# Kernel optimization log

Measured on AMD Instinct MI355X. Metric: run time of the kernel, lower is better.

Reference implementation:

```python
import jax, jax.numpy as jnp
import numpy as np

N = 100000
E = 1_600_000
IN_DIM = 128
HIDDEN = 128


def spmm(row, col, vals, H):
    # y[r] = sum_{edges e with row[e]==r} vals[e] * H[col[e]]
    msgs = vals[:, None] * H[col]          # [E, hidden] gather + scale
    return jax.ops.segment_sum(msgs, row, num_segments=H.shape[0])


def setup_inputs() -> dict:
    key = jax.random.key(0)
    ks = jax.random.split(key, 10)
    X = jax.random.normal(ks[0], (N, IN_DIM), dtype=jnp.float32)
    row = jax.random.randint(ks[1], (E,), 0, N, dtype=jnp.int32)
    col = jax.random.randint(ks[2], (E,), 0, N, dtype=jnp.int32)
    vals = jax.random.uniform(ks[3], (E,), dtype=jnp.float32)
    s_in = 1.0 / np.sqrt(IN_DIM)
    s_h = 1.0 / np.sqrt(HIDDEN)
    W_in = jax.random.normal(ks[4], (IN_DIM, HIDDEN), dtype=jnp.float32) * s_in
    b_in = jax.random.normal(ks[5], (HIDDEN,), dtype=jnp.float32) * s_in
    W_mp1 = jax.random.normal(ks[6], (HIDDEN, HIDDEN), dtype=jnp.float32) * s_h
    W_mp2 = jax.random.normal(ks[7], (HIDDEN, HIDDEN), dtype=jnp.float32) * s_h
    W_out = jax.random.normal(ks[8], (HIDDEN, 1), dtype=jnp.float32) * s_h
    b_out = jax.random.normal(ks[9], (1,), dtype=jnp.float32) * s_h
    return {"X": X, "row": row, "col": col, "vals": vals,
            "W_in": W_in, "b_in": b_in, "W_mp1": W_mp1, "W_mp2": W_mp2,
            "W_out": W_out, "b_out": b_out}


def reference(X, row, col, vals, W_in, b_in, W_mp1, W_mp2, W_out, b_out):
    H = jax.nn.relu(X @ W_in + b_in)          # [N, hidden]
    AH = spmm(row, col, vals, H)              # 1-hop propagation
    A2H = spmm(row, col, vals, AH)            # 2-hop propagation
    H2 = jax.nn.relu(AH @ W_mp1 + A2H @ W_mp2)
    return H2 @ W_out + b_out                 # [N, 1]
```

## Files before the change

### kernel.cpp

```cpp
#include <hip/hip_runtime.h>

#define N_NODES 100000
#define N_EDGES 1600000
#define NBUCK 391
#define NCHUNK 256
#define CHUNK 6250
#define LROW 136
#define DCAP 5120

typedef float f32x4 __attribute__((ext_vector_type(4)));
typedef _Float16 f16x8 __attribute__((ext_vector_type(8)));
typedef _Float16 h16x2 __attribute__((ext_vector_type(2)));

__device__ __forceinline__ unsigned f2h_bits(float f) {
    union { _Float16 h; unsigned short s; } c;
    c.h = (_Float16)f;
    return c.s;
}
__device__ __forceinline__ h16x2 u2h(unsigned u) {
    union { unsigned u; h16x2 h; } c;
    c.u = u;
    return c.h;
}
__device__ __forceinline__ unsigned pk16lo(unsigned hi, unsigned lo) {
    return __builtin_amdgcn_perm(hi, lo, 0x05040100u);
}
__device__ __forceinline__ unsigned pk16hi(unsigned hi, unsigned lo) {
    return __builtin_amdgcn_perm(hi, lo, 0x07060302u);
}
__device__ __forceinline__ float fdot2(h16x2 a, h16x2 b, float c) {
#if __has_builtin(__builtin_amdgcn_fdot2)
    return __builtin_amdgcn_fdot2(a, b, c, false);
#else
    return c + (float)a[0] * (float)b[0] + (float)a[1] * (float)b[1];
#endif
}

__device__ __forceinline__ f16x8 pack_h8(float4 a, float4 b) {
    f16x8 r;
    r[0] = (_Float16)a.x; r[1] = (_Float16)a.y;
    r[2] = (_Float16)a.z; r[3] = (_Float16)a.w;
    r[4] = (_Float16)b.x; r[5] = (_Float16)b.y;
    r[6] = (_Float16)b.z; r[7] = (_Float16)b.w;
    return r;
}


__global__ __launch_bounds__(256) void k_prep(const int* __restrict__ row,
                                              int* __restrict__ hmat,
                                              const float* __restrict__ Wa,
                                              const float* __restrict__ Wb,
                                              const float* __restrict__ Wc,
                                              unsigned short* __restrict__ Wta,
                                              unsigned short* __restrict__ Wtb,
                                              unsigned short* __restrict__ Wtc) {
    if (blockIdx.x < NCHUNK) {
        __shared__ int h[NBUCK];
        for (int i = threadIdx.x; i < NBUCK; i += 256) h[i] = 0;
        __syncthreads();
        int s = blockIdx.x * CHUNK, e = s + CHUNK;
        for (int i = s + threadIdx.x; i < e; i += 256)
            atomicAdd(&h[row[i] >> 8], 1);
        __syncthreads();
        for (int b = threadIdx.x; b < NBUCK; b += 256)
            hmat[blockIdx.x * NBUCK + b] = h[b];
    } else {
        int t = (blockIdx.x - NCHUNK) * 256 + threadIdx.x;
        int which = t >> 14;
        int i = t & 16383;
        int n = i & 127, k = i >> 7;
        const float* W = which == 0 ? Wa : which == 1 ? Wb : Wc;
        unsigned short* Wt = which == 0 ? Wta : which == 1 ? Wtb : Wtc;
        Wt[n * 128 + k] = (unsigned short)f2h_bits(W[k * 128 + n]);
    }
}

__global__ __launch_bounds__(512) void k_colscanB(const int* __restrict__ hmat,
                                                  int* __restrict__ bases,
                                                  int* __restrict__ bstart) {
    __shared__ int s[512];
    int b = blockIdx.x, t = threadIdx.x;
    if (b < NBUCK) {
        int v = (t < NCHUNK) ? hmat[t * NBUCK + b] : 0;
        s[t] = v;
        __syncthreads();
        for (int off = 1; off < 512; off <<= 1) {
            int x = (t >= off) ? s[t - off] : 0;
            __syncthreads();
            s[t] += x;
            __syncthreads();
        }
        if (t < NCHUNK) bases[t * NBUCK + b] = s[t] - v;
    } else {
        int v = 0;
        if (t < NBUCK) {
            for (int blk = 0; blk < NCHUNK; blk++) v += hmat[blk * NBUCK + t];
        }
        s[t] = v;
        __syncthreads();
        for (int off = 1; off < 512; off <<= 1) {
            int x = (t >= off) ? s[t - off] : 0;
            __syncthreads();
            s[t] += x;
            __syncthreads();
        }
        if (t < NBUCK) bstart[t] = s[t] - v;
        if (t == NBUCK) bstart[NBUCK] = N_EDGES;
    }
}

__global__ __launch_bounds__(256) void k_binC(const int* __restrict__ row,
                                              const int* __restrict__ col,
                                              const float* __restrict__ vals,
                                              const int* __restrict__ bstart,
                                              const int* __restrict__ bases,
                                              int2* __restrict__ grouped) {
    __shared__ int cnt[NBUCK];
    for (int i = threadIdx.x; i < NBUCK; i += 256) cnt[i] = 0;
    __syncthreads();
    int s = blockIdx.x * CHUNK, e = s + CHUNK;
    for (int i = s + threadIdx.x; i < e; i += 256) {
        int r = row[i];
        int b = r >> 8;
        int rank = atomicAdd(&cnt[b], 1);
        int pos = bstart[b] + bases[blockIdx.x * NBUCK + b] + rank;
        unsigned hv = f2h_bits(vals[i]);
        grouped[pos] = make_int2(col[i], ((r & 255) << 14) | hv);
    }
}

__global__ __launch_bounds__(256) void k_binD(const int2* __restrict__ grouped,
                                              const int* __restrict__ bstart,
                                              unsigned* __restrict__ evf,
                                              int* __restrict__ row_ptr) {
    __shared__ int h[256], sc[256], cur[256];
    __shared__ int2 ebuf[DCAP];
    int b = blockIdx.x, t = threadIdx.x;
    int s0 = bstart[b], e0 = bstart[b + 1];
    int n = e0 - s0;
    bool inlds = (n <= DCAP);
    h[t] = 0;
    __syncthreads();
    if (inlds) {
        for (int i = t; i < n; i += 256) ebuf[i] = grouped[s0 + i];
        __syncthreads();
        for (int i = t; i < n; i += 256)
            atomicAdd(&h[(ebuf[i].y >> 14) & 255], 1);
    } else {
        for (int i = s0 + t; i < e0; i += 256)
            atomicAdd(&h[(grouped[i].y >> 14) & 255], 1);
    }
    __syncthreads();
    int v = h[t];
    sc[t] = v;
    __syncthreads();
    for (int off = 1; off < 256; off <<= 1) {
        int x = (t >= off) ? sc[t - off] : 0;
        __syncthreads();
        sc[t] += x;
        __syncthreads();
    }
    int excl = sc[t] - v;
    cur[t] = excl;
    int grow = b * 256 + t;
    if (grow <= N_NODES) row_ptr[grow] = s0 + excl;
    __syncthreads();
    if (inlds) {
        for (int i = t; i < n; i += 256) {
            int2 g = ebuf[i];
            int rl = (g.y >> 14) & 255;
            int p = atomicAdd(&cur[rl], 1);
            evf[s0 + p] = ((unsigned)g.x << 14) | (unsigned)(g.y & 0x3fff);
        }
    } else {
        for (int i = s0 + t; i < e0; i += 256) {
            int2 g = grouped[i];
            int rl = (g.y >> 14) & 255;
            int p = atomicAdd(&cur[rl], 1);
            evf[s0 + p] = ((unsigned)g.x << 14) | (unsigned)(g.y & 0x3fff);
        }
    }
}

__global__ __launch_bounds__(256) void k_gemm_in(const float* __restrict__ X,
                                                 const unsigned short* __restrict__ Wt,
                                                 const float* __restrict__ b,
                                                 unsigned short* __restrict__ H) {
    __shared__ unsigned short lds[64 * LROW];
    int tid = threadIdx.x;
    int lane = tid & 63, wv = tid >> 6;
    int quad = lane >> 4, c16 = lane & 15;

    f16x8 wf[2][4];
    float bb[2];
#pragma unroll
    for (int nt = 0; nt < 2; nt++) {
        int ng = wv * 2 + nt;
        bb[nt] = b[ng * 16 + c16];
#pragma unroll
        for (int kc = 0; kc < 4; kc++)
            wf[nt][kc] = *(const f16x8*)&Wt[(ng * 16 + c16) * 128 + kc * 32 + quad * 8];
    }

    int tilebase = blockIdx.x * 64;
    const float4* Xg = (const float4*)X;
#pragma unroll
    for (int i = 0; i < 4; i++) {
        int c = tid + i * 256;
        int r = c >> 4, o = c & 15;
        int grow = tilebase + r;
        float4 f0 = make_float4(0.f, 0.f, 0.f, 0.f), f1 = f0;
        if (grow < N_NODES) {
            f0 = Xg[(size_t)grow * 32 + o * 2];
            f1 = Xg[(size_t)grow * 32 + o * 2 + 1];
        }
        *(f16x8*)&lds[r * LROW + o * 8] = pack_h8(f0, f1);
    }
    __syncthreads();

    f32x4 acc[4][2] = {};
#pragma unroll
    for (int t4 = 0; t4 < 4; t4++) {
#pragma unroll
        for (int kc = 0; kc < 4; kc++) {
            f16x8 af = *(const f16x8*)&lds[(t4 * 16 + c16) * LROW + kc * 32 + quad * 8];
#pragma unroll
            for (int nt = 0; nt < 2; nt++)
                acc[t4][nt] = __builtin_amdgcn_mfma_f32_16x16x32_f16(af, wf[nt][kc],
                                                                    acc[t4][nt], 0, 0, 0);
        }
    }
    __syncthreads();

#pragma unroll
    for (int t4 = 0; t4 < 4; t4++)
#pragma unroll
        for (int nt = 0; nt < 2; nt++) {
            int ncol = (wv * 2 + nt) * 16 + c16;
#pragma unroll
            for (int r = 0; r < 4; r++) {
                float v = fmaxf(acc[t4][nt][r] + bb[nt], 0.f);
                lds[(t4 * 16 + quad * 4 + r) * LROW + ncol] = (unsigned short)f2h_bits(v);
            }
        }
    __syncthreads();
#pragma unroll
    for (int i = 0; i < 4; i++) {
        int c = tid + i * 256;
        int r = c >> 4, o = c & 15;
        int grow = tilebase + r;
        if (grow < N_NODES)
            *(uint4*)&H[(size_t)grow * 128 + o * 8] = *(const uint4*)&lds[r * LROW + o * 8];
    }
}

__global__ __launch_bounds__(256) void k_spmm(const int* __restrict__ rp,
                                              const unsigned* __restrict__ evf,
                                              const unsigned* __restrict__ Hin,
                                              unsigned* __restrict__ Ho) {
    int wid = (blockIdx.x * blockDim.x + threadIdx.x) >> 6;
    int lane = threadIdx.x & 63;
    if (wid >= N_NODES) return;
    int q = lane >> 4, l16 = lane & 15;
    int s = __builtin_amdgcn_readfirstlane(rp[wid]);
    int e = __builtin_amdgcn_readfirstlane(rp[wid + 1]);
    float a0 = 0.f, a1 = 0.f, a2 = 0.f, a3 = 0.f;
    float a4 = 0.f, a5 = 0.f, a6 = 0.f, a7 = 0.f;
    for (int base = s; base < e; base += 64) {
        int cnt = e - base;
        if (cnt > 64) cnt = 64;
        unsigned ev = evf[base + (lane < cnt ? lane : cnt - 1)];
        int r = 0;
        for (; r + 16 <= cnt; r += 16) {
            unsigned u0 = __shfl(ev, r + q, 64);
            unsigned u1 = __shfl(ev, r + 4 + q, 64);
            unsigned u2 = __shfl(ev, r + 8 + q, 64);
            unsigned u3 = __shfl(ev, r + 12 + q, 64);
            const uint4 h0 = *(const uint4*)&Hin[(size_t)(u0 >> 14) * 64 + l16 * 4];
            const uint4 h1 = *(const uint4*)&Hin[(size_t)(u1 >> 14) * 64 + l16 * 4];
            const uint4 h2 = *(const uint4*)&Hin[(size_t)(u2 >> 14) * 64 + l16 * 4];
            const uint4 h3 = *(const uint4*)&Hin[(size_t)(u3 >> 14) * 64 + l16 * 4];
            h16x2 v01 = u2h(pk16lo(u1 & 0x3fffu, u0 & 0x3fffu));
            h16x2 v23 = u2h(pk16lo(u3 & 0x3fffu, u2 & 0x3fffu));
            a0 = fdot2(v01, u2h(pk16lo(h1.x, h0.x)), a0);
            a0 = fdot2(v23, u2h(pk16lo(h3.x, h2.x)), a0);
            a1 = fdot2(v01, u2h(pk16hi(h1.x, h0.x)), a1);
            a1 = fdot2(v23, u2h(pk16hi(h3.x, h2.x)), a1);
            a2 = fdot2(v01, u2h(pk16lo(h1.y, h0.y)), a2);
            a2 = fdot2(v23, u2h(pk16lo(h3.y, h2.y)), a2);
            a3 = fdot2(v01, u2h(pk16hi(h1.y, h0.y)), a3);
            a3 = fdot2(v23, u2h(pk16hi(h3.y, h2.y)), a3);
            a4 = fdot2(v01, u2h(pk16lo(h1.z, h0.z)), a4);
            a4 = fdot2(v23, u2h(pk16lo(h3.z, h2.z)), a4);
            a5 = fdot2(v01, u2h(pk16hi(h1.z, h0.z)), a5);
            a5 = fdot2(v23, u2h(pk16hi(h3.z, h2.z)), a5);
            a6 = fdot2(v01, u2h(pk16lo(h1.w, h0.w)), a6);
            a6 = fdot2(v23, u2h(pk16lo(h3.w, h2.w)), a6);
            a7 = fdot2(v01, u2h(pk16hi(h1.w, h0.w)), a7);
            a7 = fdot2(v23, u2h(pk16hi(h3.w, h2.w)), a7);
        }
        if (r < cnt) {
            int i0 = r + q, i1 = r + 4 + q, i2 = r + 8 + q, i3 = r + 12 + q;
            unsigned u0 = __shfl(ev, i0 < cnt ? i0 : cnt - 1, 64);
            unsigned u1 = __shfl(ev, i1 < cnt ? i1 : cnt - 1, 64);
            unsigned u2 = __shfl(ev, i2 < cnt ? i2 : cnt - 1, 64);
            unsigned u3 = __shfl(ev, i3 < cnt ? i3 : cnt - 1, 64);
            const uint4 h0 = *(const uint4*)&Hin[(size_t)(u0 >> 14) * 64 + l16 * 4];
            const uint4 h1 = *(const uint4*)&Hin[(size_t)(u1 >> 14) * 64 + l16 * 4];
            const uint4 h2 = *(const uint4*)&Hin[(size_t)(u2 >> 14) * 64 + l16 * 4];
            const uint4 h3 = *(const uint4*)&Hin[(size_t)(u3 >> 14) * 64 + l16 * 4];
            unsigned m0 = (i0 < cnt) ? (u0 & 0x3fffu) : 0u;
            unsigned m1 = (i1 < cnt) ? (u1 & 0x3fffu) : 0u;
            unsigned m2 = (i2 < cnt) ? (u2 & 0x3fffu) : 0u;
            unsigned m3 = (i3 < cnt) ? (u3 & 0x3fffu) : 0u;
            h16x2 v01 = u2h(pk16lo(m1, m0));
            h16x2 v23 = u2h(pk16lo(m3, m2));
            a0 = fdot2(v01, u2h(pk16lo(h1.x, h0.x)), a0);
            a0 = fdot2(v23, u2h(pk16lo(h3.x, h2.x)), a0);
            a1 = fdot2(v01, u2h(pk16hi(h1.x, h0.x)), a1);
            a1 = fdot2(v23, u2h(pk16hi(h3.x, h2.x)), a1);
            a2 = fdot2(v01, u2h(pk16lo(h1.y, h0.y)), a2);
            a2 = fdot2(v23, u2h(pk16lo(h3.y, h2.y)), a2);
            a3 = fdot2(v01, u2h(pk16hi(h1.y, h0.y)), a3);
            a3 = fdot2(v23, u2h(pk16hi(h3.y, h2.y)), a3);
            a4 = fdot2(v01, u2h(pk16lo(h1.z, h0.z)), a4);
            a4 = fdot2(v23, u2h(pk16lo(h3.z, h2.z)), a4);
            a5 = fdot2(v01, u2h(pk16hi(h1.z, h0.z)), a5);
            a5 = fdot2(v23, u2h(pk16hi(h3.z, h2.z)), a5);
            a6 = fdot2(v01, u2h(pk16lo(h1.w, h0.w)), a6);
            a6 = fdot2(v23, u2h(pk16lo(h3.w, h2.w)), a6);
            a7 = fdot2(v01, u2h(pk16hi(h1.w, h0.w)), a7);
            a7 = fdot2(v23, u2h(pk16hi(h3.w, h2.w)), a7);
        }
    }
    a0 += __shfl_xor(a0, 16, 64); a0 += __shfl_xor(a0, 32, 64);
    a1 += __shfl_xor(a1, 16, 64); a1 += __shfl_xor(a1, 32, 64);
    a2 += __shfl_xor(a2, 16, 64); a2 += __shfl_xor(a2, 32, 64);
    a3 += __shfl_xor(a3, 16, 64); a3 += __shfl_xor(a3, 32, 64);
    a4 += __shfl_xor(a4, 16, 64); a4 += __shfl_xor(a4, 32, 64);
    a5 += __shfl_xor(a5, 16, 64); a5 += __shfl_xor(a5, 32, 64);
    a6 += __shfl_xor(a6, 16, 64); a6 += __shfl_xor(a6, 32, 64);
    a7 += __shfl_xor(a7, 16, 64); a7 += __shfl_xor(a7, 32, 64);
    if (q == 0) {
        uint4 p;
        p.x = (f2h_bits(a1) << 16) | f2h_bits(a0);
        p.y = (f2h_bits(a3) << 16) | f2h_bits(a2);
        p.z = (f2h_bits(a5) << 16) | f2h_bits(a4);
        p.w = (f2h_bits(a7) << 16) | f2h_bits(a6);
        *(uint4*)&Ho[(size_t)wid * 64 + l16 * 4] = p;
    }
}

__global__ __launch_bounds__(256) void k_gemm_out(const unsigned short* __restrict__ AH,
                                                  const unsigned short* __restrict__ A2H,
                                                  const unsigned short* __restrict__ Wt1,
                                                  const unsigned short* __restrict__ Wt2,
                                                  const float* __restrict__ Wout,
                                                  const float* __restrict__ bout,
                                                  float* __restrict__ out) {
    __shared__ unsigned short lds[2][64 * LROW];
    __shared__ float part[4][64];
    int tid = threadIdx.x;
    int lane = tid & 63, wv = tid >> 6;
    int quad = lane >> 4, c16 = lane & 15;

    f16x8 w1f[2][4], w2f[2][4];
    float wo[2];
#pragma unroll
    for (int nt = 0; nt < 2; nt++) {
        int ng = wv * 2 + nt;
        wo[nt] = Wout[ng * 16 + c16];
#pragma unroll
        for (int kc = 0; kc < 4; kc++) {
            w1f[nt][kc] = *(const f16x8*)&Wt1[(ng * 16 + c16) * 128 + kc * 32 + quad * 8];
            w2f[nt][kc] = *(const f16x8*)&Wt2[(ng * 16 + c16) * 128 + kc * 32 + quad * 8];
        }
    }
    float bo = bout[0];

    int tilebase = blockIdx.x * 64;
    const uint4* Ag = (const uint4*)(AH + (size_t)tilebase * 128);
    const uint4* Bg = (const uint4*)(A2H + (size_t)tilebase * 128);
#pragma unroll
    for (int i = 0; i < 4; i++) {
        int c = tid + i * 256;
        int r = c >> 4, o = c & 15;
        *(uint4*)&lds[0][r * LROW + o * 8] = Ag[c];
        *(uint4*)&lds[1][r * LROW + o * 8] = Bg[c];
    }
    __syncthreads();

    f32x4 acc[4][2] = {};
#pragma unroll
    for (int t4 = 0; t4 < 4; t4++) {
#pragma unroll
        for (int kc = 0; kc < 4; kc++) {
            f16x8 afA = *(const f16x8*)&lds[0][(t4 * 16 + c16) * LROW + kc * 32 + quad * 8];
            f16x8 afB = *(const f16x8*)&lds[1][(t4 * 16 + c16) * LROW + kc * 32 + quad * 8];
#pragma unroll
            for (int nt = 0; nt < 2; nt++) {
                acc[t4][nt] = __builtin_amdgcn_mfma_f32_16x16x32_f16(afA, w1f[nt][kc],
                                                                    acc[t4][nt], 0, 0, 0);
                acc[t4][nt] = __builtin_amdgcn_mfma_f32_16x16x32_f16(afB, w2f[nt][kc],
                                                                    acc[t4][nt], 0, 0, 0);
            }
        }
    }

#pragma unroll
    for (int t4 = 0; t4 < 4; t4++) {
        float p[4];
#pragma unroll
        for (int r = 0; r < 4; r++)
            p[r] = fmaxf(acc[t4][0][r], 0.f) * wo[0] + fmaxf(acc[t4][1][r], 0.f) * wo[1];
#pragma unroll
        for (int m = 1; m < 16; m <<= 1)
#pragma unroll
            for (int r = 0; r < 4; r++) p[r] += __shfl_xor(p[r], m, 64);
        if (c16 == 0)
#pragma unroll
            for (int r = 0; r < 4; r++) part[wv][t4 * 16 + quad * 4 + r] = p[r];
    }
    __syncthreads();
    if (tid < 64) {
        int orow = tilebase + tid;
        if (orow < N_NODES)
            out[orow] = part[0][tid] + part[1][tid] + part[2][tid] + part[3][tid] + bo;
    }
}


extern "C" void kernel_launch(void* const* d_in, const int* in_sizes, int n_in,
                              void* d_out, int out_size, void* d_ws, size_t ws_size,
                              hipStream_t stream) {
    const float* X    = (const float*)d_in[0];
    const int*   row  = (const int*)d_in[1];
    const int*   col  = (const int*)d_in[2];
    const float* vals = (const float*)d_in[3];
    const float* W_in = (const float*)d_in[4];
    const float* b_in = (const float*)d_in[5];
    const float* W1   = (const float*)d_in[6];
    const float* W2   = (const float*)d_in[7];
    const float* Wout = (const float*)d_in[8];
    const float* bout = (const float*)d_in[9];
    float* out = (float*)d_out;

    char* ws = (char*)d_ws;
    size_t off = 0;
    auto alloc = [&](size_t bytes) -> void* {
        void* p = ws + off;
        off += (bytes + 511) & ~(size_t)511;
        return p;
    };
    unsigned short* Hb  = (unsigned short*)alloc((size_t)N_NODES * 128 * 2);
    unsigned short* AHb = (unsigned short*)alloc((size_t)N_NODES * 128 * 2);
    unsigned short* A2b = (unsigned short*)alloc((size_t)N_NODES * 128 * 2);
    unsigned* evf  = (unsigned*)alloc((size_t)N_EDGES * 4);
    int2* grouped  = (int2*)alloc((size_t)N_EDGES * 8);
    unsigned short* Wtin = (unsigned short*)alloc(128 * 128 * 2);
    unsigned short* Wt1  = (unsigned short*)alloc(128 * 128 * 2);
    unsigned short* Wt2  = (unsigned short*)alloc(128 * 128 * 2);
    int*   hmat    = (int*)alloc((size_t)NCHUNK * NBUCK * 4);
    int*   bases   = (int*)alloc((size_t)NCHUNK * NBUCK * 4);
    int*   bstart  = (int*)alloc(512 * 4);
    int*   row_ptr = (int*)alloc((size_t)(N_NODES + 256) * 4);

    k_prep<<<NCHUNK + 192, 256, 0, stream>>>(row, hmat, W_in, W1, W2, Wtin, Wt1, Wt2);
    k_colscanB<<<NBUCK + 1, 512, 0, stream>>>(hmat, bases, bstart);
    k_binC<<<NCHUNK, 256, 0, stream>>>(row, col, vals, bstart, bases, grouped);
    k_binD<<<NBUCK, 256, 0, stream>>>(grouped, bstart, evf, row_ptr);

    int gblk = (N_NODES + 63) / 64;
    k_gemm_in<<<gblk, 256, 0, stream>>>(X, Wtin, b_in, Hb);

    int sblk = (N_NODES + 3) / 4;
    k_spmm<<<sblk, 256, 0, stream>>>(row_ptr, evf, (const unsigned*)Hb, (unsigned*)AHb);
    k_spmm<<<sblk, 256, 0, stream>>>(row_ptr, evf, (const unsigned*)AHb, (unsigned*)A2b);

    k_gemm_out<<<gblk, 256, 0, stream>>>(AHb, A2b, Wt1, Wt2, Wout, bout, out);
}
```

Baseline: 305.2 us.

## Fuse input GEMM into binning kernel, use 16-lane rows in SpMM

Merges the edge-binning kernel and the input GEMM into one launch, with separate block ranges doing each job so the two independent stages overlap on the GPU. It also caches per-bucket base offsets in LDS. The second binning kernel moves to 512-thread blocks. SpMM now gives each 16-lane quarter-wave its own row instead of spreading one row over a whole wave, which removes the cross-quarter shuffle reduction. With about 16 edges per row, this should waste fewer lanes, at the cost of more divergence when row lengths differ within a wave.

```diff
diff --git a/kernel.cpp b/kernel.cpp
--- a/kernel.cpp
+++ b/kernel.cpp
@@ -109,27 +109,105 @@
     }
 }
 
-__global__ __launch_bounds__(256) void k_binC(const int* __restrict__ row,
-                                              const int* __restrict__ col,
-                                              const float* __restrict__ vals,
-                                              const int* __restrict__ bstart,
-                                              const int* __restrict__ bases,
-                                              int2* __restrict__ grouped) {
-    __shared__ int cnt[NBUCK];
-    for (int i = threadIdx.x; i < NBUCK; i += 256) cnt[i] = 0;
-    __syncthreads();
-    int s = blockIdx.x * CHUNK, e = s + CHUNK;
-    for (int i = s + threadIdx.x; i < e; i += 256) {
-        int r = row[i];
-        int b = r >> 8;
-        int rank = atomicAdd(&cnt[b], 1);
-        int pos = bstart[b] + bases[blockIdx.x * NBUCK + b] + rank;
-        unsigned hv = f2h_bits(vals[i]);
-        grouped[pos] = make_int2(col[i], ((r & 255) << 14) | hv);
-    }
-}
-
-__global__ __launch_bounds__(256) void k_binD(const int2* __restrict__ grouped,
+__global__ __launch_bounds__(256) void k_binC_gemm(const int* __restrict__ row,
+                                                   const int* __restrict__ col,
+                                                   const float* __restrict__ vals,
+                                                   const int* __restrict__ bstart,
+                                                   const int* __restrict__ bases,
+                                                   int2* __restrict__ grouped,
+                                                   const float* __restrict__ X,
+                                                   const unsigned short* __restrict__ Wt,
+                                                   const float* __restrict__ bvec,
+                                                   unsigned short* __restrict__ H) {
+    __shared__ __align__(16) char smraw[64 * LROW * 2];
+    if (blockIdx.x < NCHUNK) {
+        int* cnt = (int*)smraw;
+        int* basl = (int*)(smraw + 1600);
+        for (int i = threadIdx.x; i < NBUCK; i += 256) {
+            cnt[i] = 0;
+            basl[i] = bstart[i] + bases[blockIdx.x * NBUCK + i];
+        }
+        __syncthreads();
+        int s = blockIdx.x * CHUNK, e = s + CHUNK;
+        for (int i = s + threadIdx.x; i < e; i += 256) {
+            int r = row[i];
+            int b = r >> 8;
+            int rank = atomicAdd(&cnt[b], 1);
+            int pos = basl[b] + rank;
+            unsigned hv = f2h_bits(vals[i]);
+            grouped[pos] = make_int2(col[i], ((r & 255) << 14) | hv);
+        }
+    } else {
+        unsigned short* lds = (unsigned short*)smraw;
+        int tid = threadIdx.x;
+        int lane = tid & 63, wv = tid >> 6;
+        int quad = lane >> 4, c16 = lane & 15;
+
+        f16x8 wf[2][4];
+        float bb[2];
+#pragma unroll
+        for (int nt = 0; nt < 2; nt++) {
+            int ng = wv * 2 + nt;
+            bb[nt] = bvec[ng * 16 + c16];
+#pragma unroll
+            for (int kc = 0; kc < 4; kc++)
+                wf[nt][kc] = *(const f16x8*)&Wt[(ng * 16 + c16) * 128 + kc * 32 + quad * 8];
+        }
+
+        int tilebase = (blockIdx.x - NCHUNK) * 64;
+        const float4* Xg = (const float4*)X;
+#pragma unroll
+        for (int i = 0; i < 4; i++) {
+            int c = tid + i * 256;
+            int r = c >> 4, o = c & 15;
+            int grow = tilebase + r;
+            float4 f0 = make_float4(0.f, 0.f, 0.f, 0.f), f1 = f0;
+            if (grow < N_NODES) {
+                f0 = Xg[(size_t)grow * 32 + o * 2];
+                f1 = Xg[(size_t)grow * 32 + o * 2 + 1];
+            }
+            *(f16x8*)&lds[r * LROW + o * 8] = pack_h8(f0, f1);
+        }
+        __syncthreads();
+
+        f32x4 acc[4][2] = {};
+#pragma unroll
+        for (int t4 = 0; t4 < 4; t4++) {
+#pragma unroll
+            for (int kc = 0; kc < 4; kc++) {
+                f16x8 af = *(const f16x8*)&lds[(t4 * 16 + c16) * LROW + kc * 32 + quad * 8];
+#pragma unroll
+                for (int nt = 0; nt < 2; nt++)
+                    acc[t4][nt] = __builtin_amdgcn_mfma_f32_16x16x32_f16(af, wf[nt][kc],
+                                                                        acc[t4][nt], 0, 0, 0);
+            }
+        }
+        __syncthreads();
+
+#pragma unroll
+        for (int t4 = 0; t4 < 4; t4++)
+#pragma unroll
+            for (int nt = 0; nt < 2; nt++) {
+                int ncol = (wv * 2 + nt) * 16 + c16;
+#pragma unroll
+                for (int r = 0; r < 4; r++) {
+                    float v = fmaxf(acc[t4][nt][r] + bb[nt], 0.f);
+                    lds[(t4 * 16 + quad * 4 + r) * LROW + ncol] = (unsigned short)f2h_bits(v);
+                }
+            }
+        __syncthreads();
+#pragma unroll
+        for (int i = 0; i < 4; i++) {
+            int c = tid + i * 256;
+            int r = c >> 4, o = c & 15;
+            int grow = tilebase + r;
+            if (grow < N_NODES)
+                *(uint4*)&H[(size_t)grow * 128 + o * 8] = *(const uint4*)&lds[r * LROW + o * 8];
+        }
+    }
+}
+
+__global__ __launch_bounds__(512) void k_binD(const int2* __restrict__ grouped,
                                               const int* __restrict__ bstart,
                                               unsigned* __restrict__ evf,
                                               int* __restrict__ row_ptr) {
@@ -139,41 +217,46 @@
     int s0 = bstart[b], e0 = bstart[b + 1];
     int n = e0 - s0;
     bool inlds = (n <= DCAP);
-    h[t] = 0;
+    if (t < 256) h[t] = 0;
     __syncthreads();
     if (inlds) {
-        for (int i = t; i < n; i += 256) ebuf[i] = grouped[s0 + i];
-        __syncthreads();
-        for (int i = t; i < n; i += 256)
+        for (int i = t; i < n; i += 512) ebuf[i] = grouped[s0 + i];
+        __syncthreads();
+        for (int i = t; i < n; i += 512)
             atomicAdd(&h[(ebuf[i].y >> 14) & 255], 1);
     } else {
-        for (int i = s0 + t; i < e0; i += 256)
+        for (int i = s0 + t; i < e0; i += 512)
             atomicAdd(&h[(grouped[i].y >> 14) & 255], 1);
     }
     __syncthreads();
-    int v = h[t];
-    sc[t] = v;
+    int v = 0;
+    if (t < 256) {
+        v = h[t];
+        sc[t] = v;
+    }
     __syncthreads();
     for (int off = 1; off < 256; off <<= 1) {
-        int x = (t >= off) ? sc[t - off] : 0;
-        __syncthreads();
-        sc[t] += x;
-        __syncthreads();
-    }
-    int excl = sc[t] - v;
-    cur[t] = excl;
-    int grow = b * 256 + t;
-    if (grow <= N_NODES) row_ptr[grow] = s0 + excl;
+        int x = (t >= off && t < 256) ? sc[t - off] : 0;
+        __syncthreads();
+        if (t < 256) sc[t] += x;
+        __syncthreads();
+    }
+    if (t < 256) {
+        int excl = sc[t] - v;
+        cur[t] = excl;
+        int grow = b * 256 + t;
+        if (grow <= N_NODES) row_ptr[grow] = s0 + excl;
+    }
     __syncthreads();
     if (inlds) {
-        for (int i = t; i < n; i += 256) {
+        for (int i = t; i < n; i += 512) {
             int2 g = ebuf[i];
             int rl = (g.y >> 14) & 255;
             int p = atomicAdd(&cur[rl], 1);
             evf[s0 + p] = ((unsigned)g.x << 14) | (unsigned)(g.y & 0x3fff);
         }
     } else {
-        for (int i = s0 + t; i < e0; i += 256) {
+        for (int i = s0 + t; i < e0; i += 512) {
             int2 g = grouped[i];
             int rl = (g.y >> 14) & 255;
             int p = atomicAdd(&cur[rl], 1);
@@ -182,134 +265,34 @@
     }
 }
 
-__global__ __launch_bounds__(256) void k_gemm_in(const float* __restrict__ X,
-                                                 const unsigned short* __restrict__ Wt,
-                                                 const float* __restrict__ b,
-                                                 unsigned short* __restrict__ H) {
-    __shared__ unsigned short lds[64 * LROW];
-    int tid = threadIdx.x;
-    int lane = tid & 63, wv = tid >> 6;
-    int quad = lane >> 4, c16 = lane & 15;
-
-    f16x8 wf[2][4];
-    float bb[2];
-#pragma unroll
-    for (int nt = 0; nt < 2; nt++) {
-        int ng = wv * 2 + nt;
-        bb[nt] = b[ng * 16 + c16];
-#pragma unroll
-        for (int kc = 0; kc < 4; kc++)
-            wf[nt][kc] = *(const f16x8*)&Wt[(ng * 16 + c16) * 128 + kc * 32 + quad * 8];
-    }
-
-    int tilebase = blockIdx.x * 64;
-    const float4* Xg = (const float4*)X;
-#pragma unroll
-    for (int i = 0; i < 4; i++) {
-        int c = tid + i * 256;
-        int r = c >> 4, o = c & 15;
-        int grow = tilebase + r;
-        float4 f0 = make_float4(0.f, 0.f, 0.f, 0.f), f1 = f0;
-        if (grow < N_NODES) {
-            f0 = Xg[(size_t)grow * 32 + o * 2];
-            f1 = Xg[(size_t)grow * 32 + o * 2 + 1];
-        }
-        *(f16x8*)&lds[r * LROW + o * 8] = pack_h8(f0, f1);
-    }
-    __syncthreads();
-
-    f32x4 acc[4][2] = {};
-#pragma unroll
-    for (int t4 = 0; t4 < 4; t4++) {
-#pragma unroll
-        for (int kc = 0; kc < 4; kc++) {
-            f16x8 af = *(const f16x8*)&lds[(t4 * 16 + c16) * LROW + kc * 32 + quad * 8];
-#pragma unroll
-            for (int nt = 0; nt < 2; nt++)
-                acc[t4][nt] = __builtin_amdgcn_mfma_f32_16x16x32_f16(af, wf[nt][kc],
-                                                                    acc[t4][nt], 0, 0, 0);
-        }
-    }
-    __syncthreads();
-
-#pragma unroll
-    for (int t4 = 0; t4 < 4; t4++)
-#pragma unroll
-        for (int nt = 0; nt < 2; nt++) {
-            int ncol = (wv * 2 + nt) * 16 + c16;
-#pragma unroll
-            for (int r = 0; r < 4; r++) {
-                float v = fmaxf(acc[t4][nt][r] + bb[nt], 0.f);
-                lds[(t4 * 16 + quad * 4 + r) * LROW + ncol] = (unsigned short)f2h_bits(v);
-            }
-        }
-    __syncthreads();
-#pragma unroll
-    for (int i = 0; i < 4; i++) {
-        int c = tid + i * 256;
-        int r = c >> 4, o = c & 15;
-        int grow = tilebase + r;
-        if (grow < N_NODES)
-            *(uint4*)&H[(size_t)grow * 128 + o * 8] = *(const uint4*)&lds[r * LROW + o * 8];
-    }
-}
-
 __global__ __launch_bounds__(256) void k_spmm(const int* __restrict__ rp,
                                               const unsigned* __restrict__ evf,
                                               const unsigned* __restrict__ Hin,
                                               unsigned* __restrict__ Ho) {
-    int wid = (blockIdx.x * blockDim.x + threadIdx.x) >> 6;
-    int lane = threadIdx.x & 63;
-    if (wid >= N_NODES) return;
+    int tid = threadIdx.x;
+    int lane = tid & 63;
     int q = lane >> 4, l16 = lane & 15;
-    int s = __builtin_amdgcn_readfirstlane(rp[wid]);
-    int e = __builtin_amdgcn_readfirstlane(rp[wid + 1]);
+    int wid = (blockIdx.x * 256 + tid) >> 6;
+    int r0 = wid * 4 + q;
+    int s = rp[r0];
+    int e = rp[r0 + 1];
     float a0 = 0.f, a1 = 0.f, a2 = 0.f, a3 = 0.f;
     float a4 = 0.f, a5 = 0.f, a6 = 0.f, a7 = 0.f;
-    for (int base = s; base < e; base += 64) {
+    for (int base = s; base < e; base += 16) {
         int cnt = e - base;
-        if (cnt > 64) cnt = 64;
-        unsigned ev = evf[base + (lane < cnt ? lane : cnt - 1)];
-        int r = 0;
-        for (; r + 16 <= cnt; r += 16) {
-            unsigned u0 = __shfl(ev, r + q, 64);
-            unsigned u1 = __shfl(ev, r + 4 + q, 64);
-            unsigned u2 = __shfl(ev, r + 8 + q, 64);
-            unsigned u3 = __shfl(ev, r + 12 + q, 64);
+        if (cnt > 16) cnt = 16;
+        unsigned ev = evf[base + (l16 < cnt ? l16 : cnt - 1)];
+        for (int i = 0; i < cnt; i += 4) {
+            int i1 = i + 1, i2 = i + 2, i3 = i + 3;
+            unsigned u0 = __shfl(ev, (q << 4) + i, 64);
+            unsigned u1 = __shfl(ev, (q << 4) + (i1 < cnt ? i1 : cnt - 1), 64);
+            unsigned u2 = __shfl(ev, (q << 4) + (i2 < cnt ? i2 : cnt - 1), 64);
+            unsigned u3 = __shfl(ev, (q << 4) + (i3 < cnt ? i3 : cnt - 1), 64);
             const uint4 h0 = *(const uint4*)&Hin[(size_t)(u0 >> 14) * 64 + l16 * 4];
             const uint4 h1 = *(const uint4*)&Hin[(size_t)(u1 >> 14) * 64 + l16 * 4];
             const uint4 h2 = *(const uint4*)&Hin[(size_t)(u2 >> 14) * 64 + l16 * 4];
             const uint4 h3 = *(const uint4*)&Hin[(size_t)(u3 >> 14) * 64 + l16 * 4];
-            h16x2 v01 = u2h(pk16lo(u1 & 0x3fffu, u0 & 0x3fffu));
-            h16x2 v23 = u2h(pk16lo(u3 & 0x3fffu, u2 & 0x3fffu));
-            a0 = fdot2(v01, u2h(pk16lo(h1.x, h0.x)), a0);
-            a0 = fdot2(v23, u2h(pk16lo(h3.x, h2.x)), a0);
-            a1 = fdot2(v01, u2h(pk16hi(h1.x, h0.x)), a1);
-            a1 = fdot2(v23, u2h(pk16hi(h3.x, h2.x)), a1);
-            a2 = fdot2(v01, u2h(pk16lo(h1.y, h0.y)), a2);
-            a2 = fdot2(v23, u2h(pk16lo(h3.y, h2.y)), a2);
-            a3 = fdot2(v01, u2h(pk16hi(h1.y, h0.y)), a3);
-            a3 = fdot2(v23, u2h(pk16hi(h3.y, h2.y)), a3);
-            a4 = fdot2(v01, u2h(pk16lo(h1.z, h0.z)), a4);
-            a4 = fdot2(v23, u2h(pk16lo(h3.z, h2.z)), a4);
-            a5 = fdot2(v01, u2h(pk16hi(h1.z, h0.z)), a5);
-            a5 = fdot2(v23, u2h(pk16hi(h3.z, h2.z)), a5);
-            a6 = fdot2(v01, u2h(pk16lo(h1.w, h0.w)), a6);
-            a6 = fdot2(v23, u2h(pk16lo(h3.w, h2.w)), a6);
-            a7 = fdot2(v01, u2h(pk16hi(h1.w, h0.w)), a7);
-            a7 = fdot2(v23, u2h(pk16hi(h3.w, h2.w)), a7);
-        }
-        if (r < cnt) {
-            int i0 = r + q, i1 = r + 4 + q, i2 = r + 8 + q, i3 = r + 12 + q;
-            unsigned u0 = __shfl(ev, i0 < cnt ? i0 : cnt - 1, 64);
-            unsigned u1 = __shfl(ev, i1 < cnt ? i1 : cnt - 1, 64);
-            unsigned u2 = __shfl(ev, i2 < cnt ? i2 : cnt - 1, 64);
-            unsigned u3 = __shfl(ev, i3 < cnt ? i3 : cnt - 1, 64);
-            const uint4 h0 = *(const uint4*)&Hin[(size_t)(u0 >> 14) * 64 + l16 * 4];
-            const uint4 h1 = *(const uint4*)&Hin[(size_t)(u1 >> 14) * 64 + l16 * 4];
-            const uint4 h2 = *(const uint4*)&Hin[(size_t)(u2 >> 14) * 64 + l16 * 4];
-            const uint4 h3 = *(const uint4*)&Hin[(size_t)(u3 >> 14) * 64 + l16 * 4];
-            unsigned m0 = (i0 < cnt) ? (u0 & 0x3fffu) : 0u;
+            unsigned m0 = u0 & 0x3fffu;
             unsigned m1 = (i1 < cnt) ? (u1 & 0x3fffu) : 0u;
             unsigned m2 = (i2 < cnt) ? (u2 & 0x3fffu) : 0u;
             unsigned m3 = (i3 < cnt) ? (u3 & 0x3fffu) : 0u;
@@ -333,22 +316,12 @@
             a7 = fdot2(v23, u2h(pk16hi(h3.w, h2.w)), a7);
         }
     }
-    a0 += __shfl_xor(a0, 16, 64); a0 += __shfl_xor(a0, 32, 64);
-    a1 += __shfl_xor(a1, 16, 64); a1 += __shfl_xor(a1, 32, 64);
-    a2 += __shfl_xor(a2, 16, 64); a2 += __shfl_xor(a2, 32, 64);
-    a3 += __shfl_xor(a3, 16, 64); a3 += __shfl_xor(a3, 32, 64);
-    a4 += __shfl_xor(a4, 16, 64); a4 += __shfl_xor(a4, 32, 64);
-    a5 += __shfl_xor(a5, 16, 64); a5 += __shfl_xor(a5, 32, 64);
-    a6 += __shfl_xor(a6, 16, 64); a6 += __shfl_xor(a6, 32, 64);
-    a7 += __shfl_xor(a7, 16, 64); a7 += __shfl_xor(a7, 32, 64);
-    if (q == 0) {
-        uint4 p;
-        p.x = (f2h_bits(a1) << 16) | f2h_bits(a0);
-        p.y = (f2h_bits(a3) << 16) | f2h_bits(a2);
-        p.z = (f2h_bits(a5) << 16) | f2h_bits(a4);
-        p.w = (f2h_bits(a7) << 16) | f2h_bits(a6);
-        *(uint4*)&Ho[(size_t)wid * 64 + l16 * 4] = p;
-    }
+    uint4 p;
+    p.x = (f2h_bits(a1) << 16) | f2h_bits(a0);
+    p.y = (f2h_bits(a3) << 16) | f2h_bits(a2);
+    p.z = (f2h_bits(a5) << 16) | f2h_bits(a4);
+    p.w = (f2h_bits(a7) << 16) | f2h_bits(a6);
+    *(uint4*)&Ho[(size_t)r0 * 64 + l16 * 4] = p;
 }
 
 __global__ __launch_bounds__(256) void k_gemm_out(const unsigned short* __restrict__ AH,
@@ -465,15 +438,15 @@
     int*   bstart  = (int*)alloc(512 * 4);
     int*   row_ptr = (int*)alloc((size_t)(N_NODES + 256) * 4);
 
+    int gblk = (N_NODES + 63) / 64;
+
     k_prep<<<NCHUNK + 192, 256, 0, stream>>>(row, hmat, W_in, W1, W2, Wtin, Wt1, Wt2);
     k_colscanB<<<NBUCK + 1, 512, 0, stream>>>(hmat, bases, bstart);
-    k_binC<<<NCHUNK, 256, 0, stream>>>(row, col, vals, bstart, bases, grouped);
-    k_binD<<<NBUCK, 256, 0, stream>>>(grouped, bstart, evf, row_ptr);
-
-    int gblk = (N_NODES + 63) / 64;
-    k_gemm_in<<<gblk, 256, 0, stream>>>(X, Wtin, b_in, Hb);
-
-    int sblk = (N_NODES + 3) / 4;
+    k_binC_gemm<<<NCHUNK + gblk, 256, 0, stream>>>(row, col, vals, bstart, bases,
+                                                   grouped, X, Wtin, b_in, Hb);
+    k_binD<<<NBUCK, 512, 0, stream>>>(grouped, bstart, evf, row_ptr);
+
+    int sblk = N_NODES / 16;
     k_spmm<<<sblk, 256, 0, stream>>>(row_ptr, evf, (const unsigned*)Hb, (unsigned*)AHb);
     k_spmm<<<sblk, 256, 0, stream>>>(row_ptr, evf, (const unsigned*)AHb, (unsigned*)A2b);
 
```

After: 313.1 us. 2.6% more time.

## Replace two-pass bucket sort with global-atomic CSR build fused with input GEMM

Applied to the files above, without the earlier changes.

Replaces the four-kernel two-level bucket sort (chunk histograms, column scans, bucket binning, in-bucket sort) with a per-row global atomic histogram, a single scan kernel that builds row_ptr and cursors, and a scatter that places each edge with a global atomicAdd on its row cursor. The scatter runs in the same launch as the input GEMM, on separate blocks, so the two overlap. This removes the intermediate grouped buffer, its extra passes over memory, and two launches. In exchange it adds many contended global atomics, and edge order within each row is no longer deterministic, so floating-point sums can vary slightly between runs.

```diff
diff --git a/kernel.cpp b/kernel.cpp
--- a/kernel.cpp
+++ b/kernel.cpp
@@ -6,7 +6,7 @@
 #define NCHUNK 256
 #define CHUNK 6250
 #define LROW 136
-#define DCAP 5120
+#define SCAT 512
 
 typedef float f32x4 __attribute__((ext_vector_type(4)));
 typedef _Float16 f16x8 __attribute__((ext_vector_type(8)));
@@ -46,8 +46,9 @@
 }
 
 
-__global__ __launch_bounds__(256) void k_prep(const int* __restrict__ row,
-                                              int* __restrict__ hmat,
+__global__ __launch_bounds__(256) void k_hist(const int* __restrict__ row,
+                                              int* __restrict__ rowcnt,
+                                              int* __restrict__ btot,
                                               const float* __restrict__ Wa,
                                               const float* __restrict__ Wb,
                                               const float* __restrict__ Wc,
@@ -59,11 +60,14 @@
         for (int i = threadIdx.x; i < NBUCK; i += 256) h[i] = 0;
         __syncthreads();
         int s = blockIdx.x * CHUNK, e = s + CHUNK;
-        for (int i = s + threadIdx.x; i < e; i += 256)
-            atomicAdd(&h[row[i] >> 8], 1);
+        for (int i = s + threadIdx.x; i < e; i += 256) {
+            int r = row[i];
+            atomicAdd(&rowcnt[r], 1);
+            atomicAdd(&h[r >> 8], 1);
+        }
         __syncthreads();
         for (int b = threadIdx.x; b < NBUCK; b += 256)
-            hmat[blockIdx.x * NBUCK + b] = h[b];
+            if (h[b]) atomicAdd(&btot[b], h[b]);
     } else {
         int t = (blockIdx.x - NCHUNK) * 256 + threadIdx.x;
         int which = t >> 14;
@@ -75,83 +79,23 @@
     }
 }
 
-__global__ __launch_bounds__(512) void k_colscanB(const int* __restrict__ hmat,
-                                                  int* __restrict__ bases,
-                                                  int* __restrict__ bstart) {
-    __shared__ int s[512];
+__global__ __launch_bounds__(256) void k_scan(const int* __restrict__ rowcnt,
+                                              const int* __restrict__ btot,
+                                              int* __restrict__ row_ptr,
+                                              int* __restrict__ cursor) {
+    __shared__ int red[256], sc[256];
     int b = blockIdx.x, t = threadIdx.x;
-    if (b < NBUCK) {
-        int v = (t < NCHUNK) ? hmat[t * NBUCK + b] : 0;
-        s[t] = v;
-        __syncthreads();
-        for (int off = 1; off < 512; off <<= 1) {
-            int x = (t >= off) ? s[t - off] : 0;
-            __syncthreads();
-            s[t] += x;
-            __syncthreads();
-        }
-        if (t < NCHUNK) bases[t * NBUCK + b] = s[t] - v;
-    } else {
-        int v = 0;
-        if (t < NBUCK) {
-            for (int blk = 0; blk < NCHUNK; blk++) v += hmat[blk * NBUCK + t];
-        }
-        s[t] = v;
-        __syncthreads();
-        for (int off = 1; off < 512; off <<= 1) {
-            int x = (t >= off) ? s[t - off] : 0;
-            __syncthreads();
-            s[t] += x;
-            __syncthreads();
-        }
-        if (t < NBUCK) bstart[t] = s[t] - v;
-        if (t == NBUCK) bstart[NBUCK] = N_EDGES;
-    }
-}
-
-__global__ __launch_bounds__(256) void k_binC(const int* __restrict__ row,
-                                              const int* __restrict__ col,
-                                              const float* __restrict__ vals,
-                                              const int* __restrict__ bstart,
-                                              const int* __restrict__ bases,
-                                              int2* __restrict__ grouped) {
-    __shared__ int cnt[NBUCK];
-    for (int i = threadIdx.x; i < NBUCK; i += 256) cnt[i] = 0;
+    int part = 0;
+    for (int j = t; j < b; j += 256) part += btot[j];
+    red[t] = part;
     __syncthreads();
-    int s = blockIdx.x * CHUNK, e = s + CHUNK;
-    for (int i = s + threadIdx.x; i < e; i += 256) {
-        int r = row[i];
-        int b = r >> 8;
-        int rank = atomicAdd(&cnt[b], 1);
-        int pos = bstart[b] + bases[blockIdx.x * NBUCK + b] + rank;
-        unsigned hv = f2h_bits(vals[i]);
-        grouped[pos] = make_int2(col[i], ((r & 255) << 14) | hv);
-    }
-}
-
-__global__ __launch_bounds__(256) void k_binD(const int2* __restrict__ grouped,
-                                              const int* __restrict__ bstart,
-                                              unsigned* __restrict__ evf,
-                                              int* __restrict__ row_ptr) {
-    __shared__ int h[256], sc[256], cur[256];
-    __shared__ int2 ebuf[DCAP];
-    int b = blockIdx.x, t = threadIdx.x;
-    int s0 = bstart[b], e0 = bstart[b + 1];
-    int n = e0 - s0;
-    bool inlds = (n <= DCAP);
-    h[t] = 0;
-    __syncthreads();
-    if (inlds) {
-        for (int i = t; i < n; i += 256) ebuf[i] = grouped[s0 + i];
-        __syncthreads();
-        for (int i = t; i < n; i += 256)
-            atomicAdd(&h[(ebuf[i].y >> 14) & 255], 1);
-    } else {
-        for (int i = s0 + t; i < e0; i += 256)
-            atomicAdd(&h[(grouped[i].y >> 14) & 255], 1);
-    }
-    __syncthreads();
-    int v = h[t];
+    for (int off = 128; off > 0; off >>= 1) {
+        if (t < off) red[t] += red[t + off];
+        __syncthreads();
+    }
+    int base = red[0];
+    int grow = b * 256 + t;
+    int v = (grow < N_NODES) ? rowcnt[grow] : 0;
     sc[t] = v;
     __syncthreads();
     for (int off = 1; off < 256; off <<= 1) {
@@ -160,97 +104,98 @@
         sc[t] += x;
         __syncthreads();
     }
-    int excl = sc[t] - v;
-    cur[t] = excl;
-    int grow = b * 256 + t;
-    if (grow <= N_NODES) row_ptr[grow] = s0 + excl;
-    __syncthreads();
-    if (inlds) {
-        for (int i = t; i < n; i += 256) {
-            int2 g = ebuf[i];
-            int rl = (g.y >> 14) & 255;
-            int p = atomicAdd(&cur[rl], 1);
-            evf[s0 + p] = ((unsigned)g.x << 14) | (unsigned)(g.y & 0x3fff);
+    int excl = base + sc[t] - v;
+    if (grow < N_NODES) {
+        row_ptr[grow] = excl;
+        cursor[grow] = excl;
+    }
+    if (b == 0 && t == 0) row_ptr[N_NODES] = N_EDGES;
+}
+
+__global__ __launch_bounds__(256) void k_scatter_gemm(const int* __restrict__ row,
+                                                      const int* __restrict__ col,
+                                                      const float* __restrict__ vals,
+                                                      int* __restrict__ cursor,
+                                                      unsigned* __restrict__ evf,
+                                                      const float* __restrict__ X,
+                                                      const unsigned short* __restrict__ Wt,
+                                                      const float* __restrict__ bvec,
+                                                      unsigned short* __restrict__ H) {
+    __shared__ unsigned short lds[64 * LROW];
+    if (blockIdx.x < SCAT) {
+        int i0 = blockIdx.x * 256 + threadIdx.x;
+        for (int i = i0; i < N_EDGES; i += SCAT * 256) {
+            int r = row[i];
+            unsigned w = ((unsigned)col[i] << 14) | f2h_bits(vals[i]);
+            int p = atomicAdd(&cursor[r], 1);
+            evf[p] = w;
         }
     } else {
-        for (int i = s0 + t; i < e0; i += 256) {
-            int2 g = grouped[i];
-            int rl = (g.y >> 14) & 255;
-            int p = atomicAdd(&cur[rl], 1);
-            evf[s0 + p] = ((unsigned)g.x << 14) | (unsigned)(g.y & 0x3fff);
-        }
-    }
-}
-
-__global__ __launch_bounds__(256) void k_gemm_in(const float* __restrict__ X,
-                                                 const unsigned short* __restrict__ Wt,
-                                                 const float* __restrict__ b,
-                                                 unsigned short* __restrict__ H) {
-    __shared__ unsigned short lds[64 * LROW];
-    int tid = threadIdx.x;
-    int lane = tid & 63, wv = tid >> 6;
-    int quad = lane >> 4, c16 = lane & 15;
-
-    f16x8 wf[2][4];
-    float bb[2];
-#pragma unroll
-    for (int nt = 0; nt < 2; nt++) {
-        int ng = wv * 2 + nt;
-        bb[nt] = b[ng * 16 + c16];
-#pragma unroll
-        for (int kc = 0; kc < 4; kc++)
-            wf[nt][kc] = *(const f16x8*)&Wt[(ng * 16 + c16) * 128 + kc * 32 + quad * 8];
-    }
-
-    int tilebase = blockIdx.x * 64;
-    const float4* Xg = (const float4*)X;
-#pragma unroll
-    for (int i = 0; i < 4; i++) {
-        int c = tid + i * 256;
-        int r = c >> 4, o = c & 15;
-        int grow = tilebase + r;
-        float4 f0 = make_float4(0.f, 0.f, 0.f, 0.f), f1 = f0;
-        if (grow < N_NODES) {
-            f0 = Xg[(size_t)grow * 32 + o * 2];
-            f1 = Xg[(size_t)grow * 32 + o * 2 + 1];
-        }
-        *(f16x8*)&lds[r * LROW + o * 8] = pack_h8(f0, f1);
-    }
-    __syncthreads();
-
-    f32x4 acc[4][2] = {};
-#pragma unroll
-    for (int t4 = 0; t4 < 4; t4++) {
-#pragma unroll
-        for (int kc = 0; kc < 4; kc++) {
-            f16x8 af = *(const f16x8*)&lds[(t4 * 16 + c16) * LROW + kc * 32 + quad * 8];
-#pragma unroll
-            for (int nt = 0; nt < 2; nt++)
-                acc[t4][nt] = __builtin_amdgcn_mfma_f32_16x16x32_f16(af, wf[nt][kc],
-                                                                    acc[t4][nt], 0, 0, 0);
-        }
-    }
-    __syncthreads();
-
-#pragma unroll
-    for (int t4 = 0; t4 < 4; t4++)
+        int tid = threadIdx.x;
+        int lane = tid & 63, wv = tid >> 6;
+        int quad = lane >> 4, c16 = lane & 15;
+
+        f16x8 wf[2][4];
+        float bb[2];
 #pragma unroll
         for (int nt = 0; nt < 2; nt++) {
-            int ncol = (wv * 2 + nt) * 16 + c16;
-#pragma unroll
-            for (int r = 0; r < 4; r++) {
-                float v = fmaxf(acc[t4][nt][r] + bb[nt], 0.f);
-                lds[(t4 * 16 + quad * 4 + r) * LROW + ncol] = (unsigned short)f2h_bits(v);
+            int ng = wv * 2 + nt;
+            bb[nt] = bvec[ng * 16 + c16];
+#pragma unroll
+            for (int kc = 0; kc < 4; kc++)
+                wf[nt][kc] = *(const f16x8*)&Wt[(ng * 16 + c16) * 128 + kc * 32 + quad * 8];
+        }
+
+        int tilebase = (blockIdx.x - SCAT) * 64;
+        const float4* Xg = (const float4*)X;
+#pragma unroll
+        for (int i = 0; i < 4; i++) {
+            int c = tid + i * 256;
+            int r = c >> 4, o = c & 15;
+            int grow = tilebase + r;
+            float4 f0 = make_float4(0.f, 0.f, 0.f, 0.f), f1 = f0;
+            if (grow < N_NODES) {
+                f0 = Xg[(size_t)grow * 32 + o * 2];
+                f1 = Xg[(size_t)grow * 32 + o * 2 + 1];
             }
-        }
-    __syncthreads();
-#pragma unroll
-    for (int i = 0; i < 4; i++) {
-        int c = tid + i * 256;
-        int r = c >> 4, o = c & 15;
-        int grow = tilebase + r;
-        if (grow < N_NODES)
-            *(uint4*)&H[(size_t)grow * 128 + o * 8] = *(const uint4*)&lds[r * LROW + o * 8];
+            *(f16x8*)&lds[r * LROW + o * 8] = pack_h8(f0, f1);
+        }
+        __syncthreads();
+
+        f32x4 acc[4][2] = {};
+#pragma unroll
+        for (int t4 = 0; t4 < 4; t4++) {
+#pragma unroll
+            for (int kc = 0; kc < 4; kc++) {
+                f16x8 af = *(const f16x8*)&lds[(t4 * 16 + c16) * LROW + kc * 32 + quad * 8];
+#pragma unroll
+                for (int nt = 0; nt < 2; nt++)
+                    acc[t4][nt] = __builtin_amdgcn_mfma_f32_16x16x32_f16(af, wf[nt][kc],
+                                                                        acc[t4][nt], 0, 0, 0);
+            }
+        }
+        __syncthreads();
+
+#pragma unroll
+        for (int t4 = 0; t4 < 4; t4++)
+#pragma unroll
+            for (int nt = 0; nt < 2; nt++) {
+                int ncol = (wv * 2 + nt) * 16 + c16;
+#pragma unroll
+                for (int r = 0; r < 4; r++) {
+                    float v = fmaxf(acc[t4][nt][r] + bb[nt], 0.f);
+                    lds[(t4 * 16 + quad * 4 + r) * LROW + ncol] = (unsigned short)f2h_bits(v);
+                }
+            }
+        __syncthreads();
+#pragma unroll
+        for (int i = 0; i < 4; i++) {
+            int c = tid + i * 256;
+            int r = c >> 4, o = c & 15;
+            int grow = tilebase + r;
+            if (grow < N_NODES)
+                *(uint4*)&H[(size_t)grow * 128 + o * 8] = *(const uint4*)&lds[r * LROW + o * 8];
+        }
     }
 }
 
@@ -456,22 +401,23 @@
     unsigned short* AHb = (unsigned short*)alloc((size_t)N_NODES * 128 * 2);
     unsigned short* A2b = (unsigned short*)alloc((size_t)N_NODES * 128 * 2);
     unsigned* evf  = (unsigned*)alloc((size_t)N_EDGES * 4);
-    int2* grouped  = (int2*)alloc((size_t)N_EDGES * 8);
     unsigned short* Wtin = (unsigned short*)alloc(128 * 128 * 2);
     unsigned short* Wt1  = (unsigned short*)alloc(128 * 128 * 2);
     unsigned short* Wt2  = (unsigned short*)alloc(128 * 128 * 2);
-    int*   hmat    = (int*)alloc((size_t)NCHUNK * NBUCK * 4);
-    int*   bases   = (int*)alloc((size_t)NCHUNK * NBUCK * 4);
-    int*   bstart  = (int*)alloc(512 * 4);
-    int*   row_ptr = (int*)alloc((size_t)(N_NODES + 256) * 4);
-
-    k_prep<<<NCHUNK + 192, 256, 0, stream>>>(row, hmat, W_in, W1, W2, Wtin, Wt1, Wt2);
-    k_colscanB<<<NBUCK + 1, 512, 0, stream>>>(hmat, bases, bstart);
-    k_binC<<<NCHUNK, 256, 0, stream>>>(row, col, vals, bstart, bases, grouped);
-    k_binD<<<NBUCK, 256, 0, stream>>>(grouped, bstart, evf, row_ptr);
+    size_t zbytes = ((size_t)N_NODES + 512) * 4;
+    int* rowcnt  = (int*)alloc(zbytes);
+    int* btot    = rowcnt + N_NODES;
+    int* cursor  = (int*)alloc((size_t)N_NODES * 4);
+    int* row_ptr = (int*)alloc((size_t)(N_NODES + 256) * 4);
 
     int gblk = (N_NODES + 63) / 64;
-    k_gemm_in<<<gblk, 256, 0, stream>>>(X, Wtin, b_in, Hb);
+
+    hipMemsetAsync(rowcnt, 0, zbytes, stream);
+    k_hist<<<NCHUNK + 192, 256, 0, stream>>>(row, rowcnt, btot,
+                                             W_in, W1, W2, Wtin, Wt1, Wt2);
+    k_scan<<<NBUCK, 256, 0, stream>>>(rowcnt, btot, row_ptr, cursor);
+    k_scatter_gemm<<<SCAT + gblk, 256, 0, stream>>>(row, col, vals, cursor, evf,
+                                                    X, Wtin, b_in, Hb);
 
     int sblk = (N_NODES + 3) / 4;
     k_spmm<<<sblk, 256, 0, stream>>>(row_ptr, evf, (const unsigned*)Hb, (unsigned*)AHb);
```

Result: slower. 390.6 us (+28.0%).
